# Performance work log

Measured on AMD Instinct MI355X. Metric: run time of the kernel, lower is better.

## Reference

```python
import jax, jax.numpy as jnp
import numpy as np

L, D, H, V, BS = 12, 768, 12, 50257, 1024  # n_layer, n_embd, n_head, vocab, block_size
B, T = 2, 1024
HD = D // H
SCALE = HD ** -0.5


def setup_inputs() -> dict:
    key = jax.random.key(0)
    ks = jax.random.split(key, 10)
    s = 0.02  # init std from _init_weights
    f = lambda k, shape: jax.random.normal(k, shape, jnp.float32) * s
    return {
        "idx": jax.random.randint(ks[0], (B, T), 0, V),
        "tok_emb": f(ks[1], (V, D)),          # tied with LM head
        "pos_emb": f(ks[2], (BS, D)),
        "wqkv": f(ks[3], (L, 3 * D, D)), "bqkv": jnp.zeros((L, 3 * D), jnp.float32),
        "wproj": f(ks[4], (L, D, D)),    "bproj": jnp.zeros((L, D), jnp.float32),
        "ln1_g": jnp.ones((L, D), jnp.float32), "ln1_b": jnp.zeros((L, D), jnp.float32),
        "ln2_g": jnp.ones((L, D), jnp.float32), "ln2_b": jnp.zeros((L, D), jnp.float32),
        "w1": f(ks[5], (L, 4 * D, D)), "b1": jnp.zeros((L, 4 * D), jnp.float32),
        "w2": f(ks[6], (L, D, 4 * D)), "b2": jnp.zeros((L, D), jnp.float32),
        "lnf_g": jnp.ones((D,), jnp.float32), "lnf_b": jnp.zeros((D,), jnp.float32),
    }


def _ln(x, g, b, eps=1e-5):
    mu = jnp.mean(x, axis=-1, keepdims=True)
    var = jnp.mean(jnp.square(x - mu), axis=-1, keepdims=True)
    return (x - mu) * jax.lax.rsqrt(var + eps) * g + b


def _gpt_forward(idx, tok_emb, pos_emb, wqkv, bqkv, wproj, bproj,
                 ln1_g, ln1_b, ln2_g, ln2_b, w1, b1, w2, b2, lnf_g, lnf_b):
    Bb, Tt = idx.shape
    x = tok_emb[idx] + pos_emb[:Tt]  # [B,T,D]; dropout=0 in eval
    causal = jnp.tril(jnp.ones((Tt, Tt), bool))

    def block(x, p):
        wq, bq, wp, bp, g1, be1, g2, be2, W1, B1, W2, B2 = p
        h = _ln(x, g1, be1)
        qkv = h @ wq.T + bq                       # [B,T,3D]
        q, k, v = jnp.split(qkv, 3, axis=-1)
        to_heads = lambda z: z.reshape(Bb, Tt, H, HD).transpose(0, 2, 1, 3)
        q, k, v = to_heads(q), to_heads(k), to_heads(v)
        att = jnp.einsum('bhqd,bhkd->bhqk', q, k) * SCALE
        att = jnp.where(causal, att, -jnp.inf)
        att = jax.nn.softmax(att, axis=-1)
        y = jnp.einsum('bhqk,bhkd->bhqd', att, v)
        y = y.transpose(0, 2, 1, 3).reshape(Bb, Tt, D)
        x = x + (y @ wp.T + bp)
        h2 = _ln(x, g2, be2)
        ff = jax.nn.gelu(h2 @ W1.T + B1, approximate=False) @ W2.T + B2
        return x + ff, None

    layer_params = (wqkv, bqkv, wproj, bproj, ln1_g, ln1_b, ln2_g, ln2_b, w1, b1, w2, b2)
    x, _ = jax.lax.scan(block, x, layer_params)
    x = _ln(x, lnf_g, lnf_b)
    return x @ tok_emb.T  # tied LM head, [B,T,V]


def reference(idx, tok_emb, pos_emb, wqkv, bqkv, wproj, bproj,
              ln1_g, ln1_b, ln2_g, ln2_b, w1, b1, w2, b2, lnf_g, lnf_b):
    return _gpt_forward(idx, tok_emb, pos_emb, wqkv, bqkv, wproj, bproj,
                        ln1_g, ln1_b, ln2_g, ln2_b, w1, b1, w2, b2, lnf_g, lnf_b)
```

## Files before the change

### kernel.cpp

```cpp
#include <hip/hip_runtime.h>
#include <hip/hip_bf16.h>

#define TT 1024
#define DD 768
#define HH 12
#define LL 12
#define VV 50257
#define MROWS 2048

typedef __attribute__((ext_vector_type(4))) float f32x4;
typedef __attribute__((ext_vector_type(8))) short bf16x8;

__device__ __forceinline__ short f2bf(float f) {
  __hip_bfloat16 h = __float2bfloat16(f);
  short s;
  __builtin_memcpy(&s, &h, 2);
  return s;
}

__device__ __forceinline__ void gload16(const void* g, void* l) {
  __builtin_amdgcn_global_load_lds(
      (const __attribute__((address_space(1))) unsigned int*)g,
      (__attribute__((address_space(3))) unsigned int*)l, 16, 0, 0);
}

__device__ __forceinline__ float wsum(float v) {
#pragma unroll
  for (int o = 32; o; o >>= 1) v += __shfl_xor(v, o, 64);
  return v;
}

__global__ __launch_bounds__(256) void cvt_k(const float* __restrict__ src,
                                             short* __restrict__ dst, long n4)
{
  const long stride = (long)gridDim.x * 256;
  for (long i = (long)blockIdx.x * 256 + threadIdx.x; i < n4; i += stride) {
    const float4 v = ((const float4*)src)[i];
    short4 h;
    h.x = f2bf(v.x); h.y = f2bf(v.y); h.z = f2bf(v.z); h.w = f2bf(v.w);
    ((short4*)dst)[i] = h;
  }
}

__global__ __launch_bounds__(256) void embed_k(const int* __restrict__ idx,
    const float* __restrict__ tok, const float* __restrict__ pos,
    float* __restrict__ x)
{
  int i = blockIdx.x * 256 + threadIdx.x;
  int d = i % DD;
  int bt = i / DD;
  int t = bt & (TT - 1);
  x[i] = tok[(long)idx[bt] * DD + d] + pos[t * DD + d];
}

__global__ __launch_bounds__(256) void ln_k(const float* __restrict__ x,
    const float* __restrict__ g, const float* __restrict__ b,
    short* __restrict__ out)
{
  const int w = threadIdx.x >> 6;
  const int lane = threadIdx.x & 63;
  const int row = blockIdx.x * 4 + w;
  const float* xr = x + (long)row * DD;
  float4 v[3];
  float s = 0.f, s2 = 0.f;
#pragma unroll
  for (int i = 0; i < 3; ++i) {
    v[i] = ((const float4*)xr)[lane + i * 64];
    s  += v[i].x + v[i].y + v[i].z + v[i].w;
    s2 += v[i].x * v[i].x + v[i].y * v[i].y + v[i].z * v[i].z + v[i].w * v[i].w;
  }
  s = wsum(s); s2 = wsum(s2);
  const float mu = s * (1.f / DD);
  const float var = s2 * (1.f / DD) - mu * mu;
  const float rstd = rsqrtf(var + 1e-5f);
#pragma unroll
  for (int i = 0; i < 3; ++i) {
    const int d0 = (lane + i * 64) * 4;
    short4 h;
    h.x = f2bf((v[i].x - mu) * rstd * g[d0 + 0] + b[d0 + 0]);
    h.y = f2bf((v[i].y - mu) * rstd * g[d0 + 1] + b[d0 + 1]);
    h.z = f2bf((v[i].z - mu) * rstd * g[d0 + 2] + b[d0 + 2]);
    h.w = f2bf((v[i].w - mu) * rstd * g[d0 + 3] + b[d0 + 3]);
    ((short4*)(out + (long)row * DD))[lane + i * 64] = h;
  }
}

__global__ __launch_bounds__(256) void flash_k(const short* __restrict__ qkv,
                                               const short* __restrict__ vt,
                                               short* __restrict__ y)
{
  const int qt = (int)gridDim.x - 1 - (int)blockIdx.x;
  const int z  = blockIdx.y;
  const int zb = z / HH, zh = z % HH;
  const int w    = threadIdx.x >> 6;
  const int lane = threadIdx.x & 63;
  const int c = lane & 15, g = lane >> 4;

  __shared__ short Pl[4][16][40];
  __shared__ float Ol[4][16][64];
  __shared__ float ml[4][16], ll[4][16];

  const int qbase = qt * 16;
  const long rowQ = (long)(zb * TT + qbase + c) * (3 * DD) + zh * 64;

  bf16x8 qf[2];
  qf[0] = *(const bf16x8*)(qkv + rowQ + g * 8);
  qf[1] = *(const bf16x8*)(qkv + rowQ + 32 + g * 8);

  f32x4 O[4] = {};
  f32x4 mrun, lrun;
#pragma unroll
  for (int r = 0; r < 4; ++r) { mrun[r] = -1e30f; lrun[r] = 0.f; }

  const float CSC = 0.125f * 1.44269504089f;
  const int nt = (qbase + 15) / 32 + 1;

  for (int t = w; t < nt; t += 4) {
    const int k0 = t * 32;
    f32x4 acc[2] = {};
#pragma unroll
    for (int nf = 0; nf < 2; ++nf) {
      const long rowK = (long)(zb * TT + k0 + nf * 16 + c) * (3 * DD) + DD + zh * 64;
      bf16x8 kf0 = *(const bf16x8*)(qkv + rowK + g * 8);
      bf16x8 kf1 = *(const bf16x8*)(qkv + rowK + 32 + g * 8);
      acc[nf] = __builtin_amdgcn_mfma_f32_16x16x32_bf16(qf[0], kf0, acc[nf], 0, 0, 0);
      acc[nf] = __builtin_amdgcn_mfma_f32_16x16x32_bf16(qf[1], kf1, acc[nf], 0, 0, 0);
    }
    f32x4 tv[2];
    const int mask_needed = (k0 + 31 > qbase);
#pragma unroll
    for (int nf = 0; nf < 2; ++nf) {
      const int k_abs = k0 + nf * 16 + c;
#pragma unroll
      for (int r = 0; r < 4; ++r) {
        float val = acc[nf][r] * CSC;
        if (mask_needed && k_abs > qbase + g * 4 + r) val = -1e30f;
        tv[nf][r] = val;
      }
    }
    f32x4 rmax;
#pragma unroll
    for (int r = 0; r < 4; ++r) rmax[r] = fmaxf(tv[0][r], tv[1][r]);
#pragma unroll
    for (int off = 1; off < 16; off <<= 1) {
#pragma unroll
      for (int r = 0; r < 4; ++r) rmax[r] = fmaxf(rmax[r], __shfl_xor(rmax[r], off, 64));
    }
    f32x4 mnew, rfac;
#pragma unroll
    for (int r = 0; r < 4; ++r) {
      mnew[r] = fmaxf(mrun[r], rmax[r]);
      rfac[r] = exp2f(mrun[r] - mnew[r]);
      mrun[r] = mnew[r];
    }
    f32x4 e0, e1, rsum;
#pragma unroll
    for (int r = 0; r < 4; ++r) {
      e0[r] = exp2f(tv[0][r] - mnew[r]);
      e1[r] = exp2f(tv[1][r] - mnew[r]);
      rsum[r] = e0[r] + e1[r];
    }
#pragma unroll
    for (int off = 1; off < 16; off <<= 1) {
#pragma unroll
      for (int r = 0; r < 4; ++r) rsum[r] += __shfl_xor(rsum[r], off, 64);
    }
#pragma unroll
    for (int r = 0; r < 4; ++r) lrun[r] = lrun[r] * rfac[r] + rsum[r];
#pragma unroll
    for (int nf = 0; nf < 4; ++nf)
#pragma unroll
      for (int r = 0; r < 4; ++r) O[nf][r] *= rfac[r];
#pragma unroll
    for (int r = 0; r < 4; ++r) {
      Pl[w][g * 4 + r][c]      = f2bf(e0[r]);
      Pl[w][g * 4 + r][16 + c] = f2bf(e1[r]);
    }
    asm volatile("s_waitcnt lgkmcnt(0)" ::: "memory");
    const bf16x8 pf = *(const bf16x8*)&Pl[w][c][g * 8];
#pragma unroll
    for (int nf = 0; nf < 4; ++nf) {
      const bf16x8 vf = *(const bf16x8*)(vt + ((long)z * 64 + nf * 16 + c) * TT + k0 + g * 8);
      O[nf] = __builtin_amdgcn_mfma_f32_16x16x32_bf16(pf, vf, O[nf], 0, 0, 0);
    }
  }

#pragma unroll
  for (int nf = 0; nf < 4; ++nf)
#pragma unroll
    for (int r = 0; r < 4; ++r)
      Ol[w][g * 4 + r][nf * 16 + c] = O[nf][r];
  if (c == 0) {
#pragma unroll
    for (int r = 0; r < 4; ++r) { ml[w][g * 4 + r] = mrun[r]; ll[w][g * 4 + r] = lrun[r]; }
  }
  __syncthreads();

  for (int e = threadIdx.x; e < 16 * 64; e += 256) {
    const int row = e >> 6, d = e & 63;
    const float M = fmaxf(fmaxf(ml[0][row], ml[1][row]), fmaxf(ml[2][row], ml[3][row]));
    float L = 0.f, Ov = 0.f;
#pragma unroll
    for (int u = 0; u < 4; ++u) {
      const float f = exp2f(ml[u][row] - M);
      L += ll[u][row] * f;
      Ov += Ol[u][row][d] * f;
    }
    y[(long)(zb * TT + qbase + row) * DD + zh * 64 + d] = f2bf(Ov / L);
  }
}

template<int BM, int BN, int BK, typename TB, int EPI, bool LMSWZ, bool PIPE>
__global__ __launch_bounds__(256) void gemm_nt(
    const short* __restrict__ A, const TB* __restrict__ Bm,
    const float* __restrict__ bias, const float* __restrict__ resid,
    void* __restrict__ Cout,
    int M, int N, int K, int lda, int ldb, int ldc,
    long aSB, long aSH, long bSB, long bSH, long cSB, long cSH,
    float scale, int causal)
{
  int n0, m0;
  if constexpr (LMSWZ) {
    const int l = blockIdx.x;
    const int x = l & 7;
    const int j = l >> 3;
    const int mt = j & 15;
    const int nl = j >> 4;
    const int npan = (N + BN - 1) / BN;
    const int q = npan >> 3, rr = npan & 7;
    const int cnt = q + (x < rr);
    if (nl >= cnt) return;
    const int nstart = x * q + (x < rr ? x : rr);
    n0 = (nstart + nl) * BN;
    m0 = mt * BM;
  } else {
    n0 = blockIdx.x * BN;
    m0 = blockIdx.y * BM;
  }
  if (causal && n0 >= m0 + BM) return;
  const int z = blockIdx.z;
  const int zb = z / HH, zh = z % HH;
  const short* Ag = A + zb * aSB + zh * aSH + (long)m0 * lda;
  const TB*    Bg = Bm + zb * bSB + zh * bSH;
  const long  cOff = zb * cSB + zh * cSH;

  constexpr int NBUF = PIPE ? 2 : 1;
  __shared__ __align__(16) short Als[NBUF][BM][BK];
  __shared__ __align__(16) short Bls[NBUF][BN][BK];

  const int tid = threadIdx.x;
  const int lane = tid & 63, wid = tid >> 6;
  constexpr int WTM = BM / 2, WTN = BN / 2;
  constexpr int FM = WTM / 16, FN = WTN / 16;
  const int wr = wid >> 1, wc = wid & 1;

  f32x4 acc[FM][FN] = {};
  const int kAoff = (lane >> 4) * 8;
  constexpr bool B_IS_F32 = (sizeof(TB) == 4);
  constexpr int CPR = BK / 8;
  constexpr int NCA = BM * CPR;
  constexpr int NCB = BN * CPR;
  constexpr int IA = NCA / 256, IB = NCB / 256;
  constexpr int GPT = IA + IB;
  static_assert(CPR == 8, "swizzle assumes 128B rows (BK=64)");
  static_assert(B_IS_F32 || (NCA % 256 == 0 && NCB % 256 == 0), "chunk grid");

  auto compute = [&](int buf) {
#pragma unroll
    for (int kk = 0; kk < BK; kk += 32) {
      bf16x8 af[FM], bfr[FN];
#pragma unroll
      for (int mi = 0; mi < FM; ++mi) {
        const int Ra = wr * WTM + mi * 16 + (lane & 15);
        const int kca = (kk + kAoff) >> 3;
        af[mi] = *(const bf16x8*)&Als[buf][Ra][(kca ^ (Ra & 7)) << 3];
      }
#pragma unroll
      for (int ni = 0; ni < FN; ++ni) {
        const int Rb = wc * WTN + ni * 16 + (lane & 15);
        const int kcb = (kk + kAoff) >> 3;
        bfr[ni] = *(const bf16x8*)&Bls[buf][Rb][(kcb ^ (Rb & 7)) << 3];
      }
#pragma unroll
      for (int mi = 0; mi < FM; ++mi)
#pragma unroll
        for (int ni = 0; ni < FN; ++ni)
          acc[mi][ni] = __builtin_amdgcn_mfma_f32_16x16x32_bf16(af[mi], bfr[ni], acc[mi][ni], 0, 0, 0);
    }
  };

  if constexpr (!B_IS_F32) {
    const short* ap[IA];
    const short* bp[IB];
#pragma unroll
    for (int i = 0; i < IA; ++i) {
      const int cch = i * 256 + tid;
      const int r = cch / CPR, kc = cch % CPR;
      ap[i] = Ag + (long)r * lda + ((kc ^ (r & 7)) << 3);
    }
#pragma unroll
    for (int i = 0; i < IB; ++i) {
      const int cch = i * 256 + tid;
      const int r = cch / CPR, kc = cch % CPR;
      int gr = n0 + r; gr = (gr < N) ? gr : (N - 1);
      bp[i] = (const short*)Bg + (long)gr * ldb + ((kc ^ (r & 7)) << 3);
    }
    const int ldsoff = wid * 64 * 16;

    auto stage = [&](int buf) {
#pragma unroll
      for (int i = 0; i < IA; ++i) {
        gload16(ap[i], (char*)&Als[buf][0][0] + i * 4096 + ldsoff);
        ap[i] += BK;
      }
#pragma unroll
      for (int i = 0; i < IB; ++i) {
        gload16(bp[i], (char*)&Bls[buf][0][0] + i * 4096 + ldsoff);
        bp[i] += BK;
      }
    };

    if constexpr (PIPE) {
      const int KT = K / BK;
      stage(0);
      for (int kt = 0; kt < KT; ++kt) {
        const int cur = kt & 1;
        if (kt + 1 < KT) {
          stage(cur ^ 1);
          asm volatile("s_waitcnt vmcnt(%0)" :: "i"(GPT));
        } else {
          asm volatile("s_waitcnt vmcnt(0)");
        }
        __builtin_amdgcn_sched_barrier(0);
        __builtin_amdgcn_s_barrier();
        __builtin_amdgcn_sched_barrier(0);
        compute(cur);
        asm volatile("" ::: "memory");
        __builtin_amdgcn_s_barrier();
        __builtin_amdgcn_sched_barrier(0);
      }
    } else {
      const int KT = K / BK;
      for (int kt = 0; kt < KT; ++kt) {
        stage(0);
        __syncthreads();
        compute(0);
        __syncthreads();
      }
    }
  } else {
    for (int k0 = 0; k0 < K; k0 += BK) {
#pragma unroll
      for (int cc = tid; cc < BM * (BK / 8); cc += 256) {
        int r = cc / (BK / 8), kc = cc % (BK / 8);
        const uint4 v = *(const uint4*)(Ag + (long)r * lda + k0 + kc * 8);
        *(uint4*)((char*)&Als[0][r][0] + ((kc ^ (r & 7)) << 4)) = v;
      }
#pragma unroll
      for (int cc = tid; cc < BN * (BK / 4); cc += 256) {
        int r = cc / (BK / 4), kc = cc % (BK / 4);
        int gr = n0 + r; gr = (gr < N) ? gr : (N - 1);
        const float4 v = *(const float4*)((const float*)Bg + (long)gr * ldb + k0 + kc * 4);
        short4 h4;
        h4.x = f2bf(v.x); h4.y = f2bf(v.y); h4.z = f2bf(v.z); h4.w = f2bf(v.w);
        *(short4*)((char*)&Bls[0][r][0] + ((kc * 8) ^ ((r & 7) << 4))) = h4;
      }
      __syncthreads();
      compute(0);
      __syncthreads();
    }
  }

  const int rq = (lane >> 4) << 2;
  const int cl = lane & 15;
#pragma unroll
  for (int mi = 0; mi < FM; ++mi) {
#pragma unroll
    for (int ni = 0; ni < FN; ++ni) {
      const int cg = n0 + wc * WTN + ni * 16 + cl;
      if (cg >= N) continue;
      const int rbase = m0 + wr * WTM + mi * 16 + rq;
      if constexpr (EPI == 5) {
        if (cg >= 2 * DD) {
          const int hh = (cg - 2 * DD) >> 6, dd2 = (cg - 2 * DD) & 63;
          const int bI = rbase >> 10, tI = rbase & (TT - 1);
          const float bv = bias[cg];
          short4 h4;
          h4.x = f2bf(acc[mi][ni][0] + bv);
          h4.y = f2bf(acc[mi][ni][1] + bv);
          h4.z = f2bf(acc[mi][ni][2] + bv);
          h4.w = f2bf(acc[mi][ni][3] + bv);
          short* vtp = (short*)(void*)resid;
          *(short4*)(vtp + (((long)(bI * HH + hh) * 64 + dd2) << 10) + tI) = h4;
        } else {
#pragma unroll
          for (int q = 0; q < 4; ++q)
            ((short*)Cout)[(long)(rbase + q) * ldc + cg] = f2bf(acc[mi][ni][q] + bias[cg]);
        }
        continue;
      }
#pragma unroll
      for (int q = 0; q < 4; ++q) {
        const long cidx = cOff + (long)(rbase + q) * ldc + cg;
        const float v = acc[mi][ni][q];
        if constexpr (EPI == 0) {
          ((float*)Cout)[cidx] = v * scale;
        } else if constexpr (EPI == 1) {
          ((short*)Cout)[cidx] = f2bf(v + bias[cg]);
        } else if constexpr (EPI == 2) {
          ((float*)Cout)[cidx] = resid[cidx] + v + bias[cg];
        } else if constexpr (EPI == 3) {
          const float zz = v + bias[cg];
          ((short*)Cout)[cidx] = f2bf(0.5f * zz * (1.f + erff(zz * 0.70710678118f)));
        } else {
          ((short*)Cout)[cidx] = f2bf(v);
        }
      }
    }
  }
}

template<typename TB>
static void run_model(const int* idx, const float* tok_f, const float* pos,
                      const TB* wqkv, const float* bqkv, const TB* wproj, const float* bproj,
                      const float* ln1g, const float* ln1b, const float* ln2g, const float* ln2b,
                      const TB* w1, const float* b1, const TB* w2, const float* b2,
                      const float* lnfg, const float* lnfb, const TB* tok_w,
                      float* xa, float* xb, short* hbf, short* qkv, short* vt,
                      short* ybf, short* ffb,
                      float* out, hipStream_t stream)
{
  embed_k<<<dim3(MROWS * DD / 256), 256, 0, stream>>>(idx, tok_f, pos, xa);

  float* xc = xa;
  float* xn = xb;
  for (int l = 0; l < LL; ++l) {
    ln_k<<<dim3(MROWS / 4), 256, 0, stream>>>(xc, ln1g + l * DD, ln1b + l * DD, hbf);
    gemm_nt<128, 64, 64, TB, 5, false, true><<<dim3(36, 16, 1), 256, 0, stream>>>(
        hbf, wqkv + (long)l * 3 * DD * DD, bqkv + l * 3 * DD, (const float*)vt, qkv,
        MROWS, 3 * DD, DD, DD, DD, 3 * DD, 0, 0, 0, 0, 0, 0, 1.f, 0);
    flash_k<<<dim3(64, 24), 256, 0, stream>>>(qkv, vt, ybf);
    gemm_nt<64, 64, 64, TB, 2, false, true><<<dim3(12, 32, 1), 256, 0, stream>>>(
        ybf, wproj + (long)l * DD * DD, bproj + l * DD, xc, xn,
        MROWS, DD, DD, DD, DD, DD, 0, 0, 0, 0, 0, 0, 1.f, 0);
    ln_k<<<dim3(MROWS / 4), 256, 0, stream>>>(xn, ln2g + l * DD, ln2b + l * DD, hbf);
    gemm_nt<128, 64, 64, TB, 3, false, true><<<dim3(48, 16, 1), 256, 0, stream>>>(
        hbf, w1 + (long)l * 4 * DD * DD, b1 + l * 4 * DD, nullptr, ffb,
        MROWS, 4 * DD, DD, DD, DD, 4 * DD, 0, 0, 0, 0, 0, 0, 1.f, 0);
    gemm_nt<64, 64, 64, TB, 2, false, true><<<dim3(12, 32, 1), 256, 0, stream>>>(
        ffb, w2 + (long)l * DD * 4 * DD, b2 + l * DD, xn, xc,
        MROWS, DD, 4 * DD, 4 * DD, 4 * DD, DD, 0, 0, 0, 0, 0, 0, 1.f, 0);
  }
  ln_k<<<dim3(MROWS / 4), 256, 0, stream>>>(xc, lnfg, lnfb, hbf);
  gemm_nt<128, 128, 64, TB, 0, true, false><<<dim3(6400, 1, 1), 256, 0, stream>>>(
      hbf, tok_w, nullptr, nullptr, out,
      MROWS, VV, DD, DD, DD, VV, 0, 0, 0, 0, 0, 0, 1.f, 0);
}

extern "C" void kernel_launch(void* const* d_in, const int* in_sizes, int n_in,
                              void* d_out, int out_size, void* d_ws, size_t ws_size,
                              hipStream_t stream)
{
  const int*   idx  = (const int*)d_in[0];
  const float* tok  = (const float*)d_in[1];
  const float* pos  = (const float*)d_in[2];
  const float* wqkv = (const float*)d_in[3];
  const float* bqkv = (const float*)d_in[4];
  const float* wproj= (const float*)d_in[5];
  const float* bproj= (const float*)d_in[6];
  const float* ln1g = (const float*)d_in[7];
  const float* ln1b = (const float*)d_in[8];
  const float* ln2g = (const float*)d_in[9];
  const float* ln2b = (const float*)d_in[10];
  const float* w1   = (const float*)d_in[11];
  const float* b1   = (const float*)d_in[12];
  const float* w2   = (const float*)d_in[13];
  const float* b2   = (const float*)d_in[14];
  const float* lnfg = (const float*)d_in[15];
  const float* lnfb = (const float*)d_in[16];
  float* out = (float*)d_out;

  const long E_WQKV = (long)LL * 3 * DD * DD;
  const long E_WPRJ = (long)LL * DD * DD;
  const long E_W1   = (long)LL * 4 * DD * DD;
  const long E_W2   = E_W1;
  const long E_TOK  = (long)VV * DD;
  const long E_WSUM = E_WQKV + E_WPRJ + E_W1 + E_W2 + E_TOK;

  const size_t NEED_B = 44040192;
  const size_t NEED_A = NEED_B + 2 * (size_t)E_WSUM;

  if (ws_size < NEED_B) return;
  const bool bf16w = (ws_size >= NEED_A);

  char* ws = (char*)d_ws;
  short *wqkv_h = nullptr, *wprj_h = nullptr, *w1_h = nullptr, *w2_h = nullptr, *tok_h = nullptr;
  if (bf16w) {
    wqkv_h = (short*)ws; ws += E_WQKV * 2;
    wprj_h = (short*)ws; ws += E_WPRJ * 2;
    w1_h   = (short*)ws; ws += E_W1 * 2;
    w2_h   = (short*)ws; ws += E_W2 * 2;
    tok_h  = (short*)ws; ws += E_TOK * 2;
  }
  float* xa  = (float*)ws; ws += (size_t)MROWS * DD * 4;
  float* xb  = (float*)ws; ws += (size_t)MROWS * DD * 4;
  short* hbf = (short*)ws; ws += (size_t)MROWS * DD * 2;
  short* qkv = (short*)ws; ws += (size_t)MROWS * 3 * DD * 2;
  short* vt  = (short*)ws; ws += (size_t)24 * 64 * TT * 2;
  short* ybf = (short*)ws; ws += (size_t)MROWS * DD * 2;
  short* ffb = (short*)ws; ws += (size_t)MROWS * 4 * DD * 2;

  if (bf16w) {
    cvt_k<<<dim3(4096), 256, 0, stream>>>(wqkv, wqkv_h, E_WQKV / 4);
    cvt_k<<<dim3(4096), 256, 0, stream>>>(wproj, wprj_h, E_WPRJ / 4);
    cvt_k<<<dim3(4096), 256, 0, stream>>>(w1, w1_h, E_W1 / 4);
    cvt_k<<<dim3(4096), 256, 0, stream>>>(w2, w2_h, E_W2 / 4);
    cvt_k<<<dim3(4096), 256, 0, stream>>>(tok, tok_h, E_TOK / 4);
    run_model<short>(idx, tok, pos, wqkv_h, bqkv, wprj_h, bproj,
                     ln1g, ln1b, ln2g, ln2b, w1_h, b1, w2_h, b2, lnfg, lnfb, tok_h,
                     xa, xb, hbf, qkv, vt, ybf, ffb, out, stream);
  } else {
    run_model<float>(idx, tok, pos, wqkv, bqkv, wproj, bproj,
                     ln1g, ln1b, ln2g, ln2b, w1, b1, w2, b2, lnfg, lnfb, tok,
                     xa, xb, hbf, qkv, vt, ybf, ffb, out, stream);
  }
}
```

Before: 2.231 ms.

## Use 32x32 MFMA for LM head, widen flash key tiles, fuse weight conversions

Adds a 32x32x16 MFMA path to the GEMM template and uses it for the large tied LM-head GEMM, with a matching epilogue for the 16-register accumulator layout. The flash attention kernel now processes 64-key tiles per wave instead of 32, halving the number of softmax reduction rounds per key. The five weight-conversion launches are merged into one kernel that walks all segments. These are separate ideas: better MFMA throughput and operand reuse in the LM head, fewer serial reductions in attention, and fewer launches, at the cost of more registers and more causal-mask waste near the diagonal.

```diff
diff --git a/kernel.cpp b/kernel.cpp
--- a/kernel.cpp
+++ b/kernel.cpp
@@ -1,5 +1,6 @@
 #include <hip/hip_runtime.h>
 #include <hip/hip_bf16.h>
+#include <type_traits>
 
 #define TT 1024
 #define DD 768
@@ -9,6 +10,7 @@
 #define MROWS 2048
 
 typedef __attribute__((ext_vector_type(4))) float f32x4;
+typedef __attribute__((ext_vector_type(16))) float f32x16;
 typedef __attribute__((ext_vector_type(8))) short bf16x8;
 
 __device__ __forceinline__ short f2bf(float f) {
@@ -30,15 +32,22 @@
   return v;
 }
 
-__global__ __launch_bounds__(256) void cvt_k(const float* __restrict__ src,
-                                             short* __restrict__ dst, long n4)
+struct CvtArgs { const float* s[5]; short* d[5]; long n4[5]; };
+
+__global__ __launch_bounds__(256) void cvt5_k(CvtArgs a, long tot)
 {
   const long stride = (long)gridDim.x * 256;
-  for (long i = (long)blockIdx.x * 256 + threadIdx.x; i < n4; i += stride) {
-    const float4 v = ((const float4*)src)[i];
+  for (long i = (long)blockIdx.x * 256 + threadIdx.x; i < tot; i += stride) {
+    long off = i;
+    int s = 0;
+#pragma unroll
+    for (int q = 0; q < 4; ++q) {
+      if (off >= a.n4[s]) { off -= a.n4[s]; ++s; }
+    }
+    const float4 v = ((const float4*)a.s[s])[off];
     short4 h;
     h.x = f2bf(v.x); h.y = f2bf(v.y); h.z = f2bf(v.z); h.w = f2bf(v.w);
-    ((short4*)dst)[i] = h;
+    ((short4*)a.d[s])[off] = h;
   }
 }
 
@@ -96,7 +105,7 @@
   const int lane = threadIdx.x & 63;
   const int c = lane & 15, g = lane >> 4;
 
-  __shared__ short Pl[4][16][40];
+  __shared__ __align__(16) short Pl[4][16][72];
   __shared__ float Ol[4][16][64];
   __shared__ float ml[4][16], ll[4][16];
 
@@ -113,23 +122,23 @@
   for (int r = 0; r < 4; ++r) { mrun[r] = -1e30f; lrun[r] = 0.f; }
 
   const float CSC = 0.125f * 1.44269504089f;
-  const int nt = (qbase + 15) / 32 + 1;
+  const int nt = (qbase + 15) / 64 + 1;
 
   for (int t = w; t < nt; t += 4) {
-    const int k0 = t * 32;
-    f32x4 acc[2] = {};
-#pragma unroll
-    for (int nf = 0; nf < 2; ++nf) {
+    const int k0 = t * 64;
+    f32x4 acc[4] = {};
+#pragma unroll
+    for (int nf = 0; nf < 4; ++nf) {
       const long rowK = (long)(zb * TT + k0 + nf * 16 + c) * (3 * DD) + DD + zh * 64;
       bf16x8 kf0 = *(const bf16x8*)(qkv + rowK + g * 8);
       bf16x8 kf1 = *(const bf16x8*)(qkv + rowK + 32 + g * 8);
       acc[nf] = __builtin_amdgcn_mfma_f32_16x16x32_bf16(qf[0], kf0, acc[nf], 0, 0, 0);
       acc[nf] = __builtin_amdgcn_mfma_f32_16x16x32_bf16(qf[1], kf1, acc[nf], 0, 0, 0);
     }
-    f32x4 tv[2];
-    const int mask_needed = (k0 + 31 > qbase);
-#pragma unroll
-    for (int nf = 0; nf < 2; ++nf) {
+    f32x4 tv[4];
+    const int mask_needed = (k0 + 63 > qbase);
+#pragma unroll
+    for (int nf = 0; nf < 4; ++nf) {
       const int k_abs = k0 + nf * 16 + c;
 #pragma unroll
       for (int r = 0; r < 4; ++r) {
@@ -140,7 +149,8 @@
     }
     f32x4 rmax;
 #pragma unroll
-    for (int r = 0; r < 4; ++r) rmax[r] = fmaxf(tv[0][r], tv[1][r]);
+    for (int r = 0; r < 4; ++r)
+      rmax[r] = fmaxf(fmaxf(tv[0][r], tv[1][r]), fmaxf(tv[2][r], tv[3][r]));
 #pragma unroll
     for (int off = 1; off < 16; off <<= 1) {
 #pragma unroll
@@ -153,13 +163,16 @@
       rfac[r] = exp2f(mrun[r] - mnew[r]);
       mrun[r] = mnew[r];
     }
-    f32x4 e0, e1, rsum;
-#pragma unroll
-    for (int r = 0; r < 4; ++r) {
-      e0[r] = exp2f(tv[0][r] - mnew[r]);
-      e1[r] = exp2f(tv[1][r] - mnew[r]);
-      rsum[r] = e0[r] + e1[r];
-    }
+    f32x4 e[4], rsum;
+#pragma unroll
+    for (int r = 0; r < 4; ++r) rsum[r] = 0.f;
+#pragma unroll
+    for (int nf = 0; nf < 4; ++nf)
+#pragma unroll
+      for (int r = 0; r < 4; ++r) {
+        e[nf][r] = exp2f(tv[nf][r] - mnew[r]);
+        rsum[r] += e[nf][r];
+      }
 #pragma unroll
     for (int off = 1; off < 16; off <<= 1) {
 #pragma unroll
@@ -172,16 +185,21 @@
 #pragma unroll
       for (int r = 0; r < 4; ++r) O[nf][r] *= rfac[r];
 #pragma unroll
-    for (int r = 0; r < 4; ++r) {
-      Pl[w][g * 4 + r][c]      = f2bf(e0[r]);
-      Pl[w][g * 4 + r][16 + c] = f2bf(e1[r]);
-    }
+    for (int nf = 0; nf < 4; ++nf)
+#pragma unroll
+      for (int r = 0; r < 4; ++r)
+        Pl[w][g * 4 + r][nf * 16 + c] = f2bf(e[nf][r]);
     asm volatile("s_waitcnt lgkmcnt(0)" ::: "memory");
-    const bf16x8 pf = *(const bf16x8*)&Pl[w][c][g * 8];
+    bf16x8 pf[2];
+    pf[0] = *(const bf16x8*)&Pl[w][c][g * 8];
+    pf[1] = *(const bf16x8*)&Pl[w][c][32 + g * 8];
 #pragma unroll
     for (int nf = 0; nf < 4; ++nf) {
-      const bf16x8 vf = *(const bf16x8*)(vt + ((long)z * 64 + nf * 16 + c) * TT + k0 + g * 8);
-      O[nf] = __builtin_amdgcn_mfma_f32_16x16x32_bf16(pf, vf, O[nf], 0, 0, 0);
+      const long vrow = ((long)z * 64 + nf * 16 + c) * TT + k0;
+      const bf16x8 vf0 = *(const bf16x8*)(vt + vrow + g * 8);
+      const bf16x8 vf1 = *(const bf16x8*)(vt + vrow + 32 + g * 8);
+      O[nf] = __builtin_amdgcn_mfma_f32_16x16x32_bf16(pf[0], vf0, O[nf], 0, 0, 0);
+      O[nf] = __builtin_amdgcn_mfma_f32_16x16x32_bf16(pf[1], vf1, O[nf], 0, 0, 0);
     }
   }
 
@@ -196,8 +214,8 @@
   }
   __syncthreads();
 
-  for (int e = threadIdx.x; e < 16 * 64; e += 256) {
-    const int row = e >> 6, d = e & 63;
+  for (int e2 = threadIdx.x; e2 < 16 * 64; e2 += 256) {
+    const int row = e2 >> 6, d = e2 & 63;
     const float M = fmaxf(fmaxf(ml[0][row], ml[1][row]), fmaxf(ml[2][row], ml[3][row]));
     float L = 0.f, Ov = 0.f;
 #pragma unroll
@@ -210,7 +228,7 @@
   }
 }
 
-template<int BM, int BN, int BK, typename TB, int EPI, bool LMSWZ, bool PIPE>
+template<int BM, int BN, int BK, int MFS, typename TB, int EPI, bool LMSWZ, bool PIPE>
 __global__ __launch_bounds__(256) void gemm_nt(
     const short* __restrict__ A, const TB* __restrict__ Bm,
     const float* __restrict__ bias, const float* __restrict__ resid,
@@ -252,10 +270,15 @@
   const int lane = tid & 63, wid = tid >> 6;
   constexpr int WTM = BM / 2, WTN = BN / 2;
   constexpr int FM = WTM / 16, FN = WTN / 16;
+  constexpr int FM2 = (MFS == 32) ? WTM / 32 : 1;
+  constexpr int FN2 = (MFS == 32) ? WTN / 32 : 1;
+  constexpr int AM = (MFS == 16) ? FM : FM2;
+  constexpr int AN = (MFS == 16) ? FN : FN2;
   const int wr = wid >> 1, wc = wid & 1;
 
-  f32x4 acc[FM][FN] = {};
-  const int kAoff = (lane >> 4) * 8;
+  using accT = typename std::conditional<MFS == 16, f32x4, f32x16>::type;
+  accT acc[AM][AN] = {};
+
   constexpr bool B_IS_F32 = (sizeof(TB) == 4);
   constexpr int CPR = BK / 8;
   constexpr int NCA = BM * CPR;
@@ -266,26 +289,50 @@
   static_assert(B_IS_F32 || (NCA % 256 == 0 && NCB % 256 == 0), "chunk grid");
 
   auto compute = [&](int buf) {
-#pragma unroll
-    for (int kk = 0; kk < BK; kk += 32) {
-      bf16x8 af[FM], bfr[FN];
-#pragma unroll
-      for (int mi = 0; mi < FM; ++mi) {
-        const int Ra = wr * WTM + mi * 16 + (lane & 15);
-        const int kca = (kk + kAoff) >> 3;
-        af[mi] = *(const bf16x8*)&Als[buf][Ra][(kca ^ (Ra & 7)) << 3];
-      }
-#pragma unroll
-      for (int ni = 0; ni < FN; ++ni) {
-        const int Rb = wc * WTN + ni * 16 + (lane & 15);
-        const int kcb = (kk + kAoff) >> 3;
-        bfr[ni] = *(const bf16x8*)&Bls[buf][Rb][(kcb ^ (Rb & 7)) << 3];
-      }
-#pragma unroll
-      for (int mi = 0; mi < FM; ++mi)
-#pragma unroll
-        for (int ni = 0; ni < FN; ++ni)
-          acc[mi][ni] = __builtin_amdgcn_mfma_f32_16x16x32_bf16(af[mi], bfr[ni], acc[mi][ni], 0, 0, 0);
+    if constexpr (MFS == 16) {
+      const int kAoff = (lane >> 4) * 8;
+#pragma unroll
+      for (int kk = 0; kk < BK; kk += 32) {
+        bf16x8 af[AM], bfr[AN];
+#pragma unroll
+        for (int mi = 0; mi < AM; ++mi) {
+          const int Ra = wr * WTM + mi * 16 + (lane & 15);
+          const int kca = (kk + kAoff) >> 3;
+          af[mi] = *(const bf16x8*)&Als[buf][Ra][(kca ^ (Ra & 7)) << 3];
+        }
+#pragma unroll
+        for (int ni = 0; ni < AN; ++ni) {
+          const int Rb = wc * WTN + ni * 16 + (lane & 15);
+          const int kcb = (kk + kAoff) >> 3;
+          bfr[ni] = *(const bf16x8*)&Bls[buf][Rb][(kcb ^ (Rb & 7)) << 3];
+        }
+#pragma unroll
+        for (int mi = 0; mi < AM; ++mi)
+#pragma unroll
+          for (int ni = 0; ni < AN; ++ni)
+            acc[mi][ni] = __builtin_amdgcn_mfma_f32_16x16x32_bf16(af[mi], bfr[ni], acc[mi][ni], 0, 0, 0);
+      }
+    } else {
+#pragma unroll
+      for (int kk = 0; kk < BK; kk += 16) {
+        const int kc = (kk >> 3) + (lane >> 5);
+        bf16x8 af[AM], bfr[AN];
+#pragma unroll
+        for (int mi = 0; mi < AM; ++mi) {
+          const int Ra = wr * WTM + mi * 32 + (lane & 31);
+          af[mi] = *(const bf16x8*)&Als[buf][Ra][(kc ^ (Ra & 7)) << 3];
+        }
+#pragma unroll
+        for (int ni = 0; ni < AN; ++ni) {
+          const int Rb = wc * WTN + ni * 32 + (lane & 31);
+          bfr[ni] = *(const bf16x8*)&Bls[buf][Rb][(kc ^ (Rb & 7)) << 3];
+        }
+#pragma unroll
+        for (int mi = 0; mi < AM; ++mi)
+#pragma unroll
+          for (int ni = 0; ni < AN; ++ni)
+            acc[mi][ni] = __builtin_amdgcn_mfma_f32_32x32x16_bf16(af[mi], bfr[ni], acc[mi][ni], 0, 0, 0);
+      }
     }
   };
 
@@ -371,49 +418,80 @@
     }
   }
 
-  const int rq = (lane >> 4) << 2;
-  const int cl = lane & 15;
-#pragma unroll
-  for (int mi = 0; mi < FM; ++mi) {
-#pragma unroll
-    for (int ni = 0; ni < FN; ++ni) {
-      const int cg = n0 + wc * WTN + ni * 16 + cl;
-      if (cg >= N) continue;
-      const int rbase = m0 + wr * WTM + mi * 16 + rq;
-      if constexpr (EPI == 5) {
-        if (cg >= 2 * DD) {
-          const int hh = (cg - 2 * DD) >> 6, dd2 = (cg - 2 * DD) & 63;
-          const int bI = rbase >> 10, tI = rbase & (TT - 1);
-          const float bv = bias[cg];
-          short4 h4;
-          h4.x = f2bf(acc[mi][ni][0] + bv);
-          h4.y = f2bf(acc[mi][ni][1] + bv);
-          h4.z = f2bf(acc[mi][ni][2] + bv);
-          h4.w = f2bf(acc[mi][ni][3] + bv);
-          short* vtp = (short*)(void*)resid;
-          *(short4*)(vtp + (((long)(bI * HH + hh) * 64 + dd2) << 10) + tI) = h4;
-        } else {
-#pragma unroll
-          for (int q = 0; q < 4; ++q)
-            ((short*)Cout)[(long)(rbase + q) * ldc + cg] = f2bf(acc[mi][ni][q] + bias[cg]);
-        }
-        continue;
-      }
-#pragma unroll
-      for (int q = 0; q < 4; ++q) {
-        const long cidx = cOff + (long)(rbase + q) * ldc + cg;
-        const float v = acc[mi][ni][q];
-        if constexpr (EPI == 0) {
-          ((float*)Cout)[cidx] = v * scale;
-        } else if constexpr (EPI == 1) {
-          ((short*)Cout)[cidx] = f2bf(v + bias[cg]);
-        } else if constexpr (EPI == 2) {
-          ((float*)Cout)[cidx] = resid[cidx] + v + bias[cg];
-        } else if constexpr (EPI == 3) {
-          const float zz = v + bias[cg];
-          ((short*)Cout)[cidx] = f2bf(0.5f * zz * (1.f + erff(zz * 0.70710678118f)));
-        } else {
-          ((short*)Cout)[cidx] = f2bf(v);
+  if constexpr (MFS == 16) {
+    const int rq = (lane >> 4) << 2;
+    const int cl = lane & 15;
+#pragma unroll
+    for (int mi = 0; mi < AM; ++mi) {
+#pragma unroll
+      for (int ni = 0; ni < AN; ++ni) {
+        const int cg = n0 + wc * WTN + ni * 16 + cl;
+        if (cg >= N) continue;
+        const int rbase = m0 + wr * WTM + mi * 16 + rq;
+        if constexpr (EPI == 5) {
+          if (cg >= 2 * DD) {
+            const int hh = (cg - 2 * DD) >> 6, dd2 = (cg - 2 * DD) & 63;
+            const int bI = rbase >> 10, tI = rbase & (TT - 1);
+            const float bv = bias[cg];
+            short4 h4;
+            h4.x = f2bf(acc[mi][ni][0] + bv);
+            h4.y = f2bf(acc[mi][ni][1] + bv);
+            h4.z = f2bf(acc[mi][ni][2] + bv);
+            h4.w = f2bf(acc[mi][ni][3] + bv);
+            short* vtp = (short*)(void*)resid;
+            *(short4*)(vtp + (((long)(bI * HH + hh) * 64 + dd2) << 10) + tI) = h4;
+          } else {
+#pragma unroll
+            for (int q = 0; q < 4; ++q)
+              ((short*)Cout)[(long)(rbase + q) * ldc + cg] = f2bf(acc[mi][ni][q] + bias[cg]);
+          }
+          continue;
+        }
+#pragma unroll
+        for (int q = 0; q < 4; ++q) {
+          const long cidx = cOff + (long)(rbase + q) * ldc + cg;
+          const float v = acc[mi][ni][q];
+          if constexpr (EPI == 0) {
+            ((float*)Cout)[cidx] = v * scale;
+          } else if constexpr (EPI == 1) {
+            ((short*)Cout)[cidx] = f2bf(v + bias[cg]);
+          } else if constexpr (EPI == 2) {
+            ((float*)Cout)[cidx] = resid[cidx] + v + bias[cg];
+          } else if constexpr (EPI == 3) {
+            const float zz = v + bias[cg];
+            ((short*)Cout)[cidx] = f2bf(0.5f * zz * (1.f + erff(zz * 0.70710678118f)));
+          } else {
+            ((short*)Cout)[cidx] = f2bf(v);
+          }
+        }
+      }
+    }
+  } else {
+    const int cl = lane & 31;
+    const int rhi = (lane >> 5) * 4;
+#pragma unroll
+    for (int mi = 0; mi < AM; ++mi) {
+#pragma unroll
+      for (int ni = 0; ni < AN; ++ni) {
+        const int cg = n0 + wc * WTN + ni * 32 + cl;
+        if (cg >= N) continue;
+#pragma unroll
+        for (int reg = 0; reg < 16; ++reg) {
+          const int row = m0 + wr * WTM + mi * 32 + (reg & 3) + ((reg >> 2) * 8) + rhi;
+          const long cidx = cOff + (long)row * ldc + cg;
+          const float v = acc[mi][ni][reg];
+          if constexpr (EPI == 0) {
+            ((float*)Cout)[cidx] = v * scale;
+          } else if constexpr (EPI == 1) {
+            ((short*)Cout)[cidx] = f2bf(v + bias[cg]);
+          } else if constexpr (EPI == 2) {
+            ((float*)Cout)[cidx] = resid[cidx] + v + bias[cg];
+          } else if constexpr (EPI == 3) {
+            const float zz = v + bias[cg];
+            ((short*)Cout)[cidx] = f2bf(0.5f * zz * (1.f + erff(zz * 0.70710678118f)));
+          } else {
+            ((short*)Cout)[cidx] = f2bf(v);
+          }
         }
       }
     }
@@ -436,23 +514,23 @@
   float* xn = xb;
   for (int l = 0; l < LL; ++l) {
     ln_k<<<dim3(MROWS / 4), 256, 0, stream>>>(xc, ln1g + l * DD, ln1b + l * DD, hbf);
-    gemm_nt<128, 64, 64, TB, 5, false, true><<<dim3(36, 16, 1), 256, 0, stream>>>(
+    gemm_nt<128, 64, 64, 16, TB, 5, false, true><<<dim3(36, 16, 1), 256, 0, stream>>>(
         hbf, wqkv + (long)l * 3 * DD * DD, bqkv + l * 3 * DD, (const float*)vt, qkv,
         MROWS, 3 * DD, DD, DD, DD, 3 * DD, 0, 0, 0, 0, 0, 0, 1.f, 0);
     flash_k<<<dim3(64, 24), 256, 0, stream>>>(qkv, vt, ybf);
-    gemm_nt<64, 64, 64, TB, 2, false, true><<<dim3(12, 32, 1), 256, 0, stream>>>(
+    gemm_nt<64, 64, 64, 16, TB, 2, false, true><<<dim3(12, 32, 1), 256, 0, stream>>>(
         ybf, wproj + (long)l * DD * DD, bproj + l * DD, xc, xn,
         MROWS, DD, DD, DD, DD, DD, 0, 0, 0, 0, 0, 0, 1.f, 0);
     ln_k<<<dim3(MROWS / 4), 256, 0, stream>>>(xn, ln2g + l * DD, ln2b + l * DD, hbf);
-    gemm_nt<128, 64, 64, TB, 3, false, true><<<dim3(48, 16, 1), 256, 0, stream>>>(
+    gemm_nt<128, 64, 64, 16, TB, 3, false, true><<<dim3(48, 16, 1), 256, 0, stream>>>(
         hbf, w1 + (long)l * 4 * DD * DD, b1 + l * 4 * DD, nullptr, ffb,
         MROWS, 4 * DD, DD, DD, DD, 4 * DD, 0, 0, 0, 0, 0, 0, 1.f, 0);
-    gemm_nt<64, 64, 64, TB, 2, false, true><<<dim3(12, 32, 1), 256, 0, stream>>>(
+    gemm_nt<64, 64, 64, 16, TB, 2, false, true><<<dim3(12, 32, 1), 256, 0, stream>>>(
         ffb, w2 + (long)l * DD * 4 * DD, b2 + l * DD, xn, xc,
         MROWS, DD, 4 * DD, 4 * DD, 4 * DD, DD, 0, 0, 0, 0, 0, 0, 1.f, 0);
   }
   ln_k<<<dim3(MROWS / 4), 256, 0, stream>>>(xc, lnfg, lnfb, hbf);
-  gemm_nt<128, 128, 64, TB, 0, true, false><<<dim3(6400, 1, 1), 256, 0, stream>>>(
+  gemm_nt<128, 128, 64, 32, TB, 0, true, false><<<dim3(6400, 1, 1), 256, 0, stream>>>(
       hbf, tok_w, nullptr, nullptr, out,
       MROWS, VV, DD, DD, DD, VV, 0, 0, 0, 0, 0, 0, 1.f, 0);
 }
@@ -511,11 +589,14 @@
   short* ffb = (short*)ws; ws += (size_t)MROWS * 4 * DD * 2;
 
   if (bf16w) {
-    cvt_k<<<dim3(4096), 256, 0, stream>>>(wqkv, wqkv_h, E_WQKV / 4);
-    cvt_k<<<dim3(4096), 256, 0, stream>>>(wproj, wprj_h, E_WPRJ / 4);
-    cvt_k<<<dim3(4096), 256, 0, stream>>>(w1, w1_h, E_W1 / 4);
-    cvt_k<<<dim3(4096), 256, 0, stream>>>(w2, w2_h, E_W2 / 4);
-    cvt_k<<<dim3(4096), 256, 0, stream>>>(tok, tok_h, E_TOK / 4);
+    CvtArgs ca;
+    ca.s[0] = wqkv; ca.d[0] = wqkv_h; ca.n4[0] = E_WQKV / 4;
+    ca.s[1] = wproj; ca.d[1] = wprj_h; ca.n4[1] = E_WPRJ / 4;
+    ca.s[2] = w1;   ca.d[2] = w1_h;   ca.n4[2] = E_W1 / 4;
+    ca.s[3] = w2;   ca.d[3] = w2_h;   ca.n4[3] = E_W2 / 4;
+    ca.s[4] = tok;  ca.d[4] = tok_h;  ca.n4[4] = E_TOK / 4;
+    const long tot = (E_WQKV + E_WPRJ + E_W1 + E_W2 + E_TOK) / 4;
+    cvt5_k<<<dim3(4096), 256, 0, stream>>>(ca, tot);
     run_model<short>(idx, tok, pos, wqkv_h, bqkv, wprj_h, bproj,
                      ln1g, ln1b, ln2g, ln2b, w1_h, b1, w2_h, b2, lnfg, lnfb, tok_h,
                      xa, xb, hbf, qkv, vt, ybf, ffb, out, stream);
```

Result: no change. 2.253 ms (+1.0%).
